# Performance work log

Measured on AMD Instinct MI355X. Metric: run time of the kernel, lower is better.

## Reference

```python
import jax, jax.numpy as jnp
import numpy as np


def _cross_head_proj(x, sw, qw1, qw2, kw1, kw2, qdd, kdd):
    # x: [B,N,T,S] attention logits/probs; sw: [N,N]
    # qw1/qw2: [B,T,I,N], kw1/kw2: [B,S,I,N] (I=2 dynamic rank), qdd: [B,T,N], kdd: [B,S,N]
    out = x + jnp.einsum('bnts,nm->bmts', x, sw)
    # low-rank dynamic mixing along query positions (sum over i reproduces the range(2) loop)
    qh = jnp.einsum('bnts,btin->bits', x, qw1)          # [B,I,T,S]
    out = out + jnp.einsum('bits,btin->bnts', qh, qw2)
    # low-rank dynamic mixing along key positions
    kh = jnp.einsum('bnts,bsin->bits', x, kw1)          # [B,I,T,S]
    out = out + jnp.einsum('bits,bsin->bnts', kh, kw2)
    # diagonal (per-head) dynamic terms
    out = out + x * jnp.transpose(qdd, (0, 2, 1))[:, :, :, None]   # [B,N,T,1]
    out = out + x * jnp.transpose(kdd, (0, 2, 1))[:, :, None, :]   # [B,N,1,S]
    return out


def setup_inputs() -> dict:
    key = jax.random.key(0)
    ks = jax.random.split(key, 18)
    B, N, T, S, D, I = 1, 32, 1024, 1024, 128, 2
    scale = 0.05  # dynamic weights come out of tanh/RMSnorm in the original; keep them small
    query = jax.random.normal(ks[0], (B, N, T, D), jnp.float32) * (D ** -0.5)
    k_ = jax.random.normal(ks[1], (B, N, S, D), jnp.float32)
    v_ = jax.random.normal(ks[2], (B, N, S, D), jnp.float32)
    neg = jnp.finfo(jnp.float32).min * 0.5  # matches make_causal_mask
    atten_mask = jnp.where(jnp.arange(S)[None, :] <= jnp.arange(T)[:, None], 0.0, neg).astype(jnp.float32)
    def dws(i0):
        return (
            jax.random.normal(ks[i0 + 0], (N, N), jnp.float32) * scale,
            jax.random.normal(ks[i0 + 1], (B, T, I, N), jnp.float32) * scale,
            jax.random.normal(ks[i0 + 2], (B, T, I, N), jnp.float32) * scale,
            jax.random.normal(ks[i0 + 3], (B, S, I, N), jnp.float32) * scale,
            jax.random.normal(ks[i0 + 4], (B, S, I, N), jnp.float32) * scale,
            jax.random.normal(ks[i0 + 5], (B, T, N), jnp.float32) * scale,
            jax.random.normal(ks[i0 + 6], (B, S, N), jnp.float32) * scale,
        )
    sw_pre, qw1_pre, qw2_pre, kw1_pre, kw2_pre, qdd_pre, kdd_pre = dws(3)
    sw_post, qw1_post, qw2_post, kw1_post, kw2_post, qdd_post, kdd_post = dws(10)
    return {
        'query': query, 'key': k_, 'value': v_, 'atten_mask': atten_mask,
        'sw_pre': sw_pre, 'qw1_pre': qw1_pre, 'qw2_pre': qw2_pre, 'kw1_pre': kw1_pre,
        'kw2_pre': kw2_pre, 'qdd_pre': qdd_pre, 'kdd_pre': kdd_pre,
        'sw_post': sw_post, 'qw1_post': qw1_post, 'qw2_post': qw2_post, 'kw1_post': kw1_post,
        'kw2_post': kw2_post, 'qdd_post': qdd_post, 'kdd_post': kdd_post,
    }


def reference(query, key, value, atten_mask,
              sw_pre, qw1_pre, qw2_pre, kw1_pre, kw2_pre, qdd_pre, kdd_pre,
              sw_post, qw1_post, qw2_post, kw1_post, kw2_post, qdd_post, kdd_post):
    # _atten_context: QK^T -> pre cross-head proj -> mask -> softmax -> post cross-head proj -> AV
    logits = jnp.einsum('bntd,bnsd->bnts', query, key)
    logits = _cross_head_proj(logits, sw_pre, qw1_pre, qw2_pre, kw1_pre, kw2_pre, qdd_pre, kdd_pre)
    logits = logits + atten_mask  # [T,S] broadcasts over [B,N,T,S]
    probs = jax.nn.softmax(logits, axis=-1)
    probs = _cross_head_proj(probs, sw_post, qw1_post, qw2_post, kw1_post, kw2_post, qdd_post, kdd_post)
    return jnp.einsum('bnts,bnsd->bntd', probs, value)
```

## Files before the change

kernel.cpp:

```cpp
#include <hip/hip_runtime.h>
#include <hip/hip_bf16.h>
#include <cstdint>
#include <cstddef>

#define T_DIM 1024
#define S_DIM 1024
#define N_HEADS 32
#define D_HEAD 128

typedef __attribute__((ext_vector_type(8))) short short8;
typedef __attribute__((ext_vector_type(4))) float floatx4;

__device__ inline int pack_bf16(float a, float b) {
    __hip_bfloat162 h = __float22bfloat162_rn(make_float2(a, b));
    int r; __builtin_memcpy(&r, &h, 4); return r;
}
__device__ inline ushort f2b(float x) {
    __hip_bfloat16 h = __float2bfloat16(x);
    ushort u; __builtin_memcpy(&u, &h, 2); return u;
}
__device__ inline float b2f(ushort u) {
    unsigned int v = ((unsigned int)u) << 16;
    float f; __builtin_memcpy(&f, &v, 4); return f;
}

__global__ __launch_bounds__(256) void tobf16(const float* __restrict__ Q,
                                              const float* __restrict__ K,
                                              ushort* __restrict__ Qb,
                                              ushort* __restrict__ Kb) {
    const size_t gid = (size_t)blockIdx.x * 256 + threadIdx.x;
    #pragma unroll
    for (int j = 0; j < 2; ++j) {
        size_t i = gid + (size_t)j * 524288;
        float4 q = ((const float4*)Q)[i];
        int2 qp; qp.x = pack_bf16(q.x, q.y); qp.y = pack_bf16(q.z, q.w);
        ((int2*)Qb)[i] = qp;
        float4 k = ((const float4*)K)[i];
        int2 kp; kp.x = pack_bf16(k.x, k.y); kp.y = pack_bf16(k.z, k.w);
        ((int2*)Kb)[i] = kp;
    }
}

__global__ __launch_bounds__(256) void vt_kernel(const float* __restrict__ V,
                                                 ushort* __restrict__ Vt) {
    const int s0 = blockIdx.x * 64;
    const int n  = blockIdx.y;
    __shared__ float lds[128 * 65];

    const int tid = threadIdx.x;
    const float* Vn = V + ((size_t)n * S_DIM + s0) * D_HEAD;

    #pragma unroll
    for (int it = 0; it < 8; ++it) {
        int idx = tid + it * 256;
        int d4 = idx & 31, s = idx >> 5;
        float4 v = *(const float4*)(Vn + (size_t)s * D_HEAD + d4 * 4);
        lds[(d4 * 4 + 0) * 65 + s] = v.x;
        lds[(d4 * 4 + 1) * 65 + s] = v.y;
        lds[(d4 * 4 + 2) * 65 + s] = v.z;
        lds[(d4 * 4 + 3) * 65 + s] = v.w;
    }
    __syncthreads();

    ushort* Vtn = Vt + (size_t)n * D_HEAD * S_DIM;
    #pragma unroll
    for (int it = 0; it < 4; ++it) {
        int idx = tid + it * 256;
        int sg = idx & 7, d = idx >> 3;
        const float* src = &lds[d * 65 + sg * 8];
        int4 o;
        o.x = pack_bf16(src[0], src[1]);
        o.y = pack_bf16(src[2], src[3]);
        o.z = pack_bf16(src[4], src[5]);
        o.w = pack_bf16(src[6], src[7]);
        *(int4*)&Vtn[(size_t)d * S_DIM + s0 + sg * 8] = o;
    }
}

__global__ __launch_bounds__(256, 2) void qk2(const ushort* __restrict__ Qb,
                                              const ushort* __restrict__ Kb,
                                              ushort* __restrict__ Lb) {
    const int bid  = blockIdx.x;
    const int xcd  = bid & 7;
    const int i    = bid >> 3;
    const int st   = i & 15;
    const int pair = (i >> 4) * 8 + xcd;
    const int n    = pair >> 4;
    const int tt   = pair & 15;
    if (st > tt) return;

    __shared__ int Qt[64 * 64];
    __shared__ int Kt[64 * 64];

    const int tid = threadIdx.x;
    const int wv = tid >> 6, ln = tid & 63;
    const int frow = ln & 15, quad = ln >> 4;

    const ushort* Qn = Qb + ((size_t)n * T_DIM + (size_t)tt * 64) * D_HEAD;
    const ushort* Kn = Kb + ((size_t)n * S_DIM + (size_t)st * 64) * D_HEAD;

    #pragma unroll
    for (int rep = 0; rep < 8; ++rep) {
        int idx = (tid + rep * 256) & 1023;
        int row = idx >> 4;
        int c   = idx & 15;
        int kb  = c >> 2, qw = c & 3;
        int dst = row * 64 + kb * 16 + ((qw * 4) ^ (4 * (row & 3)));
        if (rep < 4) {
            uint4 v = *(const uint4*)(Qn + (size_t)row * D_HEAD + c * 8);
            *(uint4*)&Qt[dst] = v;
        } else {
            uint4 v = *(const uint4*)(Kn + (size_t)row * D_HEAD + c * 8);
            *(uint4*)&Kt[dst] = v;
        }
    }
    __syncthreads();

    const int swz = 4 * (frow & 3);
    floatx4 acc[4] = {};
    #pragma unroll
    for (int kb = 0; kb < 4; ++kb) {
        const short8 af = *(const short8*)&Qt[(wv * 16 + frow) * 64 + kb * 16 + ((quad * 4) ^ swz)];
        #pragma unroll
        for (int si = 0; si < 4; ++si) {
            const short8 bf = *(const short8*)&Kt[(si * 16 + frow) * 64 + kb * 16 + ((quad * 4) ^ swz)];
            acc[si] = __builtin_amdgcn_mfma_f32_16x16x32_bf16(af, bf, acc[si], 0, 0, 0);
        }
    }
    __syncthreads();

    ushort* Ot = (ushort*)Qt;
    #pragma unroll
    for (int si = 0; si < 4; ++si)
        #pragma unroll
        for (int r = 0; r < 4; ++r)
            Ot[(wv * 16 + quad * 4 + r) * 72 + si * 16 + frow] = f2b(acc[si][r]);
    __syncthreads();

    #pragma unroll
    for (int it = 0; it < 2; ++it) {
        int idx = tid + it * 256;
        int row = idx >> 3, col = idx & 7;
        int4 v = *(const int4*)&Ot[row * 72 + col * 8];
        *(int4*)&Lb[((size_t)n * T_DIM + tt * 64 + row) * S_DIM + st * 64 + col * 8] = v;
    }
}

__global__ __launch_bounds__(256) void mat4_kernel(
        const float* __restrict__ sw_pre,  const float* __restrict__ qw1_pre,
        const float* __restrict__ qw2_pre, const float* __restrict__ qdd_pre,
        const float* __restrict__ kw1_pre, const float* __restrict__ kw2_pre,
        const float* __restrict__ kdd_pre,
        const float* __restrict__ sw_post,  const float* __restrict__ qw1_post,
        const float* __restrict__ qw2_post, const float* __restrict__ qdd_post,
        const float* __restrict__ kw1_post, const float* __restrict__ kw2_post,
        const float* __restrict__ kdd_post,
        ushort* __restrict__ mats) {
    const float *sw, *w1, *w2, *dd;
    float idadd;
    switch (blockIdx.y) {
        case 0:  sw = sw_pre;  w1 = qw1_pre;  w2 = qw2_pre;  dd = qdd_pre;  idadd = 1.0f; break;
        case 1:  sw = nullptr; w1 = kw1_pre;  w2 = kw2_pre;  dd = kdd_pre;  idadd = 0.0f; break;
        case 2:  sw = sw_post; w1 = qw1_post; w2 = qw2_post; dd = qdd_post; idadd = 1.0f; break;
        default: sw = nullptr; w1 = kw1_post; w2 = kw2_post; dd = kdd_post; idadd = 0.0f; break;
    }
    ushort* out = mats + (size_t)blockIdx.y * 1024 * 1024;

    const int t = blockIdx.x;
    const int tid = threadIdx.x;
    const int m = tid >> 3;
    const int n0 = (tid & 7) * 4;

    const float w2m0 = w2[t * 64 + m];
    const float w2m1 = w2[t * 64 + 32 + m];
    const float ddm  = dd[t * 32 + m];

    float v[4];
    #pragma unroll
    for (int j = 0; j < 4; ++j) {
        int n = n0 + j;
        float r = w1[t * 64 + n] * w2m0 + w1[t * 64 + 32 + n] * w2m1;
        if (sw) r += sw[n * 32 + m];
        if (n == m) r += idadd + ddm;
        v[j] = r;
    }
    int p0 = pack_bf16(v[0], v[1]);
    int p1 = pack_bf16(v[2], v[3]);
    int2 st = make_int2(p0, p1);
    *(int2*)&out[(size_t)t * 1024 + m * 32 + n0] = st;
}

template<bool SM>
__global__ __launch_bounds__(256, 4) void proj6(ushort* __restrict__ Lb,
                                                const ushort* __restrict__ Cmat,
                                                const ushort* __restrict__ Kmat,
                                                const float2* __restrict__ stats2,
                                                float2* __restrict__ pstat) {
    const int bid = blockIdx.y * 64 + blockIdx.x;
    const int xcd = bid & 7;
    const int idx = bid >> 3;
    const int ty  = ((idx >> 6) << 3) + xcd;
    const int sx  = idx & 63;

    const int s0 = sx * 16;
    const int t0 = ty * 16;
    if (s0 > t0 + 15) return;

    __shared__ __align__(16) ushort Xs[16 * 648];
    __shared__ __align__(16) float  Kp[16 * 260];

    const int tid = threadIdx.x;
    const int wv = tid >> 6, ln = tid & 63;
    const int frow = ln & 15, quad = ln >> 4;

    #pragma unroll
    for (int it = 0; it < 4; ++it) {
        int slot = tid + it * 256;
        int c    = slot & 1;
        int row  = slot >> 1;
        int nn   = row >> 4, tl = row & 15;
        uint4 ld = *(const uint4*)(Lb + ((size_t)nn * T_DIM + t0 + tl) * S_DIM + s0 + c * 8);
        ushort u[8];
        u[0] = (ushort)(ld.x & 0xffff);  u[1] = (ushort)(ld.x >> 16);
        u[2] = (ushort)(ld.y & 0xffff);  u[3] = (ushort)(ld.y >> 16);
        u[4] = (ushort)(ld.z & 0xffff);  u[5] = (ushort)(ld.z >> 16);
        u[6] = (ushort)(ld.w & 0xffff);  u[7] = (ushort)(ld.w >> 16);
        if (SM) {
            const float2 ms = stats2[(t0 + tl) * 32 + nn];
            const int tG = t0 + tl, sbase = s0 + c * 8;
            #pragma unroll
            for (int j = 0; j < 8; ++j) {
                float x = (sbase + j <= tG) ? __expf(b2f(u[j]) - ms.x) * ms.y : 0.0f;
                u[j] = f2b(x);
            }
        }
        ushort* xp = &Xs[tl * 648 + (c * 8) * 40 + nn];
        #pragma unroll
        for (int j = 0; j < 8; ++j) xp[j * 40] = u[j];
    }
    __syncthreads();

    #pragma unroll
    for (int mh = 0; mh < 2; ++mh) {
        #pragma unroll
        for (int k = 0; k < 4; ++k) {
            const int sl = wv * 4 + k;
            const short8 af = *(const short8*)(Kmat + (size_t)(s0 + sl) * 1024 + (mh * 16 + frow) * 32 + quad * 8);
            const short8 bf = *(const short8*)&Xs[frow * 648 + sl * 40 + quad * 8];
            floatx4 z = {0.f, 0.f, 0.f, 0.f};
            floatx4 d = __builtin_amdgcn_mfma_f32_16x16x32_bf16(af, bf, z, 0, 0, 0);
            *(floatx4*)&Kp[frow * 260 + sl * 16 + quad * 4] = d;
        }
        __syncthreads();

        #pragma unroll
        for (int i = 0; i < 4; ++i) {
            const int tl = wv * 4 + i;
            const int tg = t0 + tl;
            const short8 bf = *(const short8*)(Cmat + (size_t)tg * 1024 + (mh * 16 + frow) * 32 + quad * 8);
            const short8 af = *(const short8*)&Xs[tl * 648 + frow * 40 + quad * 8];
            floatx4 z = {0.f, 0.f, 0.f, 0.f};
            floatx4 d = __builtin_amdgcn_mfma_f32_16x16x32_bf16(af, bf, z, 0, 0, 0);
            float v[4];
            float lm = -INFINITY, lsum = 0.0f;
            #pragma unroll
            for (int r = 0; r < 4; ++r) {
                const int sl = quad * 4 + r;
                float val = d[r] + Kp[tl * 260 + sl * 16 + frow];
                const bool ok = (s0 + sl <= tg);
                v[r] = ok ? val : 0.0f;
                if (!SM) lm = fmaxf(lm, ok ? val : -INFINITY);
            }
            if (!SM) {
                #pragma unroll
                for (int r = 0; r < 4; ++r) {
                    const int sl = quad * 4 + r;
                    if (s0 + sl <= tg) lsum += __expf(v[r] - lm);
                }
                #pragma unroll
                for (int off = 16; off <= 32; off <<= 1) {
                    float om = __shfl_xor(lm, off);
                    float os = __shfl_xor(lsum, off);
                    float nm = fmaxf(lm, om);
                    float a = (lm > -1e37f) ? lsum * __expf(lm - nm) : 0.0f;
                    float b = (om > -1e37f) ? os   * __expf(om - nm) : 0.0f;
                    lm = nm; lsum = a + b;
                }
                if (quad == 0)
                    pstat[((size_t)tg * 64 + sx) * 32 + mh * 16 + frow] = make_float2(lm, lsum);
            }
            uint2 stv;
            stv.x = (unsigned)pack_bf16(v[0], v[1]);
            stv.y = (unsigned)pack_bf16(v[2], v[3]);
            *(uint2*)&Lb[((size_t)(mh * 16 + frow) * T_DIM + tg) * S_DIM + s0 + quad * 4] = stv;
        }
        __syncthreads();
    }
}

__global__ __launch_bounds__(256) void statreduce(const float2* __restrict__ pstat,
                                                  float2* __restrict__ stats2) {
    const int t = blockIdx.x;
    const int ty = t >> 4;
    const int total = (ty + 1) * 32;
    __shared__ float sm[32][65];
    __shared__ float ss[32][65];

    const int tid = threadIdx.x;
    for (int base = 0; base < total; base += 256) {
        int idx = base + tid;
        if (idx < total) {
            float2 p = pstat[(size_t)t * 2048 + idx];
            sm[idx & 31][idx >> 5] = p.x;
            ss[idx & 31][idx >> 5] = p.y;
        }
    }
    __syncthreads();

    const int n = tid >> 3, j = tid & 7;
    float m = -INFINITY, s = 0.0f;
    for (int sx = j; sx <= ty; sx += 8) {
        float om = sm[n][sx], os = ss[n][sx];
        float nm = fmaxf(m, om);
        float a = (m  > -1e37f) ? s  * __expf(m  - nm) : 0.0f;
        float b = (om > -1e37f) ? os * __expf(om - nm) : 0.0f;
        m = nm; s = a + b;
    }
    #pragma unroll
    for (int off = 1; off < 8; off <<= 1) {
        float om = __shfl_xor(m, off);
        float os = __shfl_xor(s, off);
        float nm = fmaxf(m, om);
        float a = (m  > -1e37f) ? s  * __expf(m  - nm) : 0.0f;
        float b = (om > -1e37f) ? os * __expf(om - nm) : 0.0f;
        m = nm; s = a + b;
    }
    if (j == 0) stats2[t * 32 + n] = make_float2(m, 1.0f / s);
}

__global__ __launch_bounds__(256, 3) void av4(const ushort* __restrict__ P,
                                              const ushort* __restrict__ Vt,
                                              float* __restrict__ O) {
    const int tid = threadIdx.x;
    const int wv = tid >> 6, ln = tid & 63;
    const int frow = ln & 15, quad = ln >> 4;
    const int n  = blockIdx.x;
    const int tt = 31 - blockIdx.y;
    const int t0 = tt * 32;

    __shared__ ushort red[4][32][136];

    const ushort* Pn  = P  + ((size_t)n * T_DIM + t0) * S_DIM;
    const ushort* Vtn = Vt + (size_t)n * D_HEAD * S_DIM;

    const int nsteps  = tt + 1;
    const int nclean0 = t0 >> 5;
    const int nclean1 = (t0 + 16) >> 5;

    floatx4 acc[2][8] = {};
    for (int sb = wv; sb < nsteps; sb += 4) {
        const int scol = sb * 32 + quad * 8;
        short8 a0 = *(const short8*)(Pn + (size_t)frow * S_DIM + scol);
        short8 a1 = *(const short8*)(Pn + (size_t)(16 + frow) * S_DIM + scol);
        if (sb >= nclean0) {
            const int tg = t0 + frow;
            #pragma unroll
            for (int j = 0; j < 8; ++j)
                if (scol + j > tg) a0[j] = 0;
        }
        if (sb >= nclean1) {
            const int tg = t0 + 16 + frow;
            #pragma unroll
            for (int j = 0; j < 8; ++j)
                if (scol + j > tg) a1[j] = 0;
        }
        #pragma unroll
        for (int dc = 0; dc < 8; ++dc) {
            const short8 b = *(const short8*)(Vtn + (size_t)(dc * 16 + frow) * S_DIM + sb * 32 + quad * 8);
            acc[0][dc] = __builtin_amdgcn_mfma_f32_16x16x32_bf16(a0, b, acc[0][dc], 0, 0, 0);
            acc[1][dc] = __builtin_amdgcn_mfma_f32_16x16x32_bf16(a1, b, acc[1][dc], 0, 0, 0);
        }
    }

    #pragma unroll
    for (int tq = 0; tq < 2; ++tq)
        #pragma unroll
        for (int dc = 0; dc < 8; ++dc)
            #pragma unroll
            for (int r = 0; r < 4; ++r)
                red[wv][tq * 16 + quad * 4 + r][dc * 16 + frow] = f2b(acc[tq][dc][r]);
    __syncthreads();

    #pragma unroll
    for (int it = 0; it < 4; ++it) {
        int idx = tid + it * 256;
        int d4 = idx & 31, tr = idx >> 5;
        float4 v;
        v.x = b2f(red[0][tr][d4 * 4 + 0]) + b2f(red[1][tr][d4 * 4 + 0]) + b2f(red[2][tr][d4 * 4 + 0]) + b2f(red[3][tr][d4 * 4 + 0]);
        v.y = b2f(red[0][tr][d4 * 4 + 1]) + b2f(red[1][tr][d4 * 4 + 1]) + b2f(red[2][tr][d4 * 4 + 1]) + b2f(red[3][tr][d4 * 4 + 1]);
        v.z = b2f(red[0][tr][d4 * 4 + 2]) + b2f(red[1][tr][d4 * 4 + 2]) + b2f(red[2][tr][d4 * 4 + 2]) + b2f(red[3][tr][d4 * 4 + 2]);
        v.w = b2f(red[0][tr][d4 * 4 + 3]) + b2f(red[1][tr][d4 * 4 + 3]) + b2f(red[2][tr][d4 * 4 + 3]) + b2f(red[3][tr][d4 * 4 + 3]);
        *(float4*)&O[((size_t)n * T_DIM + t0 + tr) * D_HEAD + d4 * 4] = v;
    }
}

extern "C" void kernel_launch(void* const* d_in, const int* in_sizes, int n_in,
                              void* d_out, int out_size, void* d_ws, size_t ws_size,
                              hipStream_t stream) {
    const float* Q    = (const float*)d_in[0];
    const float* K    = (const float*)d_in[1];
    const float* V    = (const float*)d_in[2];
    const float* sw_pre  = (const float*)d_in[4];
    const float* qw1_pre = (const float*)d_in[5];
    const float* qw2_pre = (const float*)d_in[6];
    const float* kw1_pre = (const float*)d_in[7];
    const float* kw2_pre = (const float*)d_in[8];
    const float* qdd_pre = (const float*)d_in[9];
    const float* kdd_pre = (const float*)d_in[10];
    const float* sw_post  = (const float*)d_in[11];
    const float* qw1_post = (const float*)d_in[12];
    const float* qw2_post = (const float*)d_in[13];
    const float* kw1_post = (const float*)d_in[14];
    const float* kw2_post = (const float*)d_in[15];
    const float* qdd_post = (const float*)d_in[16];
    const float* kdd_post = (const float*)d_in[17];

    ushort* Lb = (ushort*)d_ws;
    ushort* Vt = (ushort*)((char*)d_ws + (size_t)64 * 1024 * 1024);
    ushort* Qb = (ushort*)((char*)d_ws + (size_t)72 * 1024 * 1024);
    ushort* Kb = (ushort*)((char*)d_ws + (size_t)80 * 1024 * 1024);
    float2* pstat = (float2*)((char*)d_ws + (size_t)96 * 1024 * 1024);
    float*  O  = (float*)d_out;

    ushort* mats  = (ushort*)d_out;
    ushort* Cpre  = mats + 0 * 1024 * 1024;
    ushort* Kpre  = mats + 1 * 1024 * 1024;
    ushort* Cpost = mats + 2 * 1024 * 1024;
    ushort* Kpost = mats + 3 * 1024 * 1024;
    float2* stats2 = (float2*)((char*)d_out + (size_t)8 * 1024 * 1024);

    mat4_kernel<<<dim3(1024, 4), 256, 0, stream>>>(
        sw_pre, qw1_pre, qw2_pre, qdd_pre, kw1_pre, kw2_pre, kdd_pre,
        sw_post, qw1_post, qw2_post, qdd_post, kw1_post, kw2_post, kdd_post, mats);
    tobf16<<<dim3(2048), 256, 0, stream>>>(Q, K, Qb, Kb);
    vt_kernel<<<dim3(16, 32), 256, 0, stream>>>(V, Vt);

    qk2<<<dim3(8192), 256, 0, stream>>>(Qb, Kb, Lb);
    proj6<false><<<dim3(64, 64), 256, 0, stream>>>(Lb, Cpre, Kpre, nullptr, pstat);
    statreduce<<<dim3(1024), 256, 0, stream>>>(pstat, stats2);
    proj6<true><<<dim3(64, 64), 256, 0, stream>>>(Lb, Cpost, Kpost, stats2, nullptr);
    av4<<<dim3(32, 32), 256, 0, stream>>>(Lb, Vt, O);
}
```

Measured before the change: 244.6 us.

## Merge prep kernels into one launch and compute two K tiles per QK block

The three preprocessing kernels (mixing-matrix build, Q/K bf16 conversion, V transpose) become a single launch that dispatches on block index. This removes two kernel launches and their gaps. The QK^T kernel now has each block reuse its staged Q tile across two adjacent 64-wide K tiles, which halves the grid and the Q reloads. In exchange it uses more LDS per block (three tiles) and adds a conditional second tile at the causal diagonal, with the occupancy hint raised to 3.

```diff
diff --git a/kernel.cpp b/kernel.cpp
--- a/kernel.cpp
+++ b/kernel.cpp
@@ -24,129 +24,9 @@
     float f; __builtin_memcpy(&f, &v, 4); return f;
 }
 
-__global__ __launch_bounds__(256) void tobf16(const float* __restrict__ Q,
-                                              const float* __restrict__ K,
-                                              ushort* __restrict__ Qb,
-                                              ushort* __restrict__ Kb) {
-    const size_t gid = (size_t)blockIdx.x * 256 + threadIdx.x;
-    #pragma unroll
-    for (int j = 0; j < 2; ++j) {
-        size_t i = gid + (size_t)j * 524288;
-        float4 q = ((const float4*)Q)[i];
-        int2 qp; qp.x = pack_bf16(q.x, q.y); qp.y = pack_bf16(q.z, q.w);
-        ((int2*)Qb)[i] = qp;
-        float4 k = ((const float4*)K)[i];
-        int2 kp; kp.x = pack_bf16(k.x, k.y); kp.y = pack_bf16(k.z, k.w);
-        ((int2*)Kb)[i] = kp;
-    }
-}
-
-__global__ __launch_bounds__(256) void vt_kernel(const float* __restrict__ V,
-                                                 ushort* __restrict__ Vt) {
-    const int s0 = blockIdx.x * 64;
-    const int n  = blockIdx.y;
-    __shared__ float lds[128 * 65];
-
-    const int tid = threadIdx.x;
-    const float* Vn = V + ((size_t)n * S_DIM + s0) * D_HEAD;
-
-    #pragma unroll
-    for (int it = 0; it < 8; ++it) {
-        int idx = tid + it * 256;
-        int d4 = idx & 31, s = idx >> 5;
-        float4 v = *(const float4*)(Vn + (size_t)s * D_HEAD + d4 * 4);
-        lds[(d4 * 4 + 0) * 65 + s] = v.x;
-        lds[(d4 * 4 + 1) * 65 + s] = v.y;
-        lds[(d4 * 4 + 2) * 65 + s] = v.z;
-        lds[(d4 * 4 + 3) * 65 + s] = v.w;
-    }
-    __syncthreads();
-
-    ushort* Vtn = Vt + (size_t)n * D_HEAD * S_DIM;
-    #pragma unroll
-    for (int it = 0; it < 4; ++it) {
-        int idx = tid + it * 256;
-        int sg = idx & 7, d = idx >> 3;
-        const float* src = &lds[d * 65 + sg * 8];
-        int4 o;
-        o.x = pack_bf16(src[0], src[1]);
-        o.y = pack_bf16(src[2], src[3]);
-        o.z = pack_bf16(src[4], src[5]);
-        o.w = pack_bf16(src[6], src[7]);
-        *(int4*)&Vtn[(size_t)d * S_DIM + s0 + sg * 8] = o;
-    }
-}
-
-__global__ __launch_bounds__(256, 2) void qk2(const ushort* __restrict__ Qb,
-                                              const ushort* __restrict__ Kb,
-                                              ushort* __restrict__ Lb) {
-    const int bid  = blockIdx.x;
-    const int xcd  = bid & 7;
-    const int i    = bid >> 3;
-    const int st   = i & 15;
-    const int pair = (i >> 4) * 8 + xcd;
-    const int n    = pair >> 4;
-    const int tt   = pair & 15;
-    if (st > tt) return;
-
-    __shared__ int Qt[64 * 64];
-    __shared__ int Kt[64 * 64];
-
-    const int tid = threadIdx.x;
-    const int wv = tid >> 6, ln = tid & 63;
-    const int frow = ln & 15, quad = ln >> 4;
-
-    const ushort* Qn = Qb + ((size_t)n * T_DIM + (size_t)tt * 64) * D_HEAD;
-    const ushort* Kn = Kb + ((size_t)n * S_DIM + (size_t)st * 64) * D_HEAD;
-
-    #pragma unroll
-    for (int rep = 0; rep < 8; ++rep) {
-        int idx = (tid + rep * 256) & 1023;
-        int row = idx >> 4;
-        int c   = idx & 15;
-        int kb  = c >> 2, qw = c & 3;
-        int dst = row * 64 + kb * 16 + ((qw * 4) ^ (4 * (row & 3)));
-        if (rep < 4) {
-            uint4 v = *(const uint4*)(Qn + (size_t)row * D_HEAD + c * 8);
-            *(uint4*)&Qt[dst] = v;
-        } else {
-            uint4 v = *(const uint4*)(Kn + (size_t)row * D_HEAD + c * 8);
-            *(uint4*)&Kt[dst] = v;
-        }
-    }
-    __syncthreads();
-
-    const int swz = 4 * (frow & 3);
-    floatx4 acc[4] = {};
-    #pragma unroll
-    for (int kb = 0; kb < 4; ++kb) {
-        const short8 af = *(const short8*)&Qt[(wv * 16 + frow) * 64 + kb * 16 + ((quad * 4) ^ swz)];
-        #pragma unroll
-        for (int si = 0; si < 4; ++si) {
-            const short8 bf = *(const short8*)&Kt[(si * 16 + frow) * 64 + kb * 16 + ((quad * 4) ^ swz)];
-            acc[si] = __builtin_amdgcn_mfma_f32_16x16x32_bf16(af, bf, acc[si], 0, 0, 0);
-        }
-    }
-    __syncthreads();
-
-    ushort* Ot = (ushort*)Qt;
-    #pragma unroll
-    for (int si = 0; si < 4; ++si)
-        #pragma unroll
-        for (int r = 0; r < 4; ++r)
-            Ot[(wv * 16 + quad * 4 + r) * 72 + si * 16 + frow] = f2b(acc[si][r]);
-    __syncthreads();
-
-    #pragma unroll
-    for (int it = 0; it < 2; ++it) {
-        int idx = tid + it * 256;
-        int row = idx >> 3, col = idx & 7;
-        int4 v = *(const int4*)&Ot[row * 72 + col * 8];
-        *(int4*)&Lb[((size_t)n * T_DIM + tt * 64 + row) * S_DIM + st * 64 + col * 8] = v;
-    }
-}
-
-__global__ __launch_bounds__(256) void mat4_kernel(
+__global__ __launch_bounds__(256) void prep(
+        const float* __restrict__ Q, const float* __restrict__ K,
+        const float* __restrict__ V,
         const float* __restrict__ sw_pre,  const float* __restrict__ qw1_pre,
         const float* __restrict__ qw2_pre, const float* __restrict__ qdd_pre,
         const float* __restrict__ kw1_pre, const float* __restrict__ kw2_pre,
@@ -155,39 +35,163 @@
         const float* __restrict__ qw2_post, const float* __restrict__ qdd_post,
         const float* __restrict__ kw1_post, const float* __restrict__ kw2_post,
         const float* __restrict__ kdd_post,
-        ushort* __restrict__ mats) {
-    const float *sw, *w1, *w2, *dd;
-    float idadd;
-    switch (blockIdx.y) {
-        case 0:  sw = sw_pre;  w1 = qw1_pre;  w2 = qw2_pre;  dd = qdd_pre;  idadd = 1.0f; break;
-        case 1:  sw = nullptr; w1 = kw1_pre;  w2 = kw2_pre;  dd = kdd_pre;  idadd = 0.0f; break;
-        case 2:  sw = sw_post; w1 = qw1_post; w2 = qw2_post; dd = qdd_post; idadd = 1.0f; break;
-        default: sw = nullptr; w1 = kw1_post; w2 = kw2_post; dd = kdd_post; idadd = 0.0f; break;
-    }
-    ushort* out = mats + (size_t)blockIdx.y * 1024 * 1024;
-
-    const int t = blockIdx.x;
+        ushort* __restrict__ mats, ushort* __restrict__ Qb,
+        ushort* __restrict__ Kb, ushort* __restrict__ Vt) {
+    __shared__ float lds[128 * 65];
+    const int bid = blockIdx.x;
     const int tid = threadIdx.x;
-    const int m = tid >> 3;
-    const int n0 = (tid & 7) * 4;
-
-    const float w2m0 = w2[t * 64 + m];
-    const float w2m1 = w2[t * 64 + 32 + m];
-    const float ddm  = dd[t * 32 + m];
-
-    float v[4];
-    #pragma unroll
-    for (int j = 0; j < 4; ++j) {
-        int n = n0 + j;
-        float r = w1[t * 64 + n] * w2m0 + w1[t * 64 + 32 + n] * w2m1;
-        if (sw) r += sw[n * 32 + m];
-        if (n == m) r += idadd + ddm;
-        v[j] = r;
-    }
-    int p0 = pack_bf16(v[0], v[1]);
-    int p1 = pack_bf16(v[2], v[3]);
-    int2 st = make_int2(p0, p1);
-    *(int2*)&out[(size_t)t * 1024 + m * 32 + n0] = st;
+
+    if (bid < 4096) {
+        const int fam = bid & 3;
+        const int t   = bid >> 2;
+        const float *sw, *w1, *w2, *dd;
+        float idadd;
+        switch (fam) {
+            case 0:  sw = sw_pre;  w1 = qw1_pre;  w2 = qw2_pre;  dd = qdd_pre;  idadd = 1.0f; break;
+            case 1:  sw = nullptr; w1 = kw1_pre;  w2 = kw2_pre;  dd = kdd_pre;  idadd = 0.0f; break;
+            case 2:  sw = sw_post; w1 = qw1_post; w2 = qw2_post; dd = qdd_post; idadd = 1.0f; break;
+            default: sw = nullptr; w1 = kw1_post; w2 = kw2_post; dd = kdd_post; idadd = 0.0f; break;
+        }
+        ushort* out = mats + (size_t)fam * 1024 * 1024;
+        const int m = tid >> 3;
+        const int n0 = (tid & 7) * 4;
+        const float w2m0 = w2[t * 64 + m];
+        const float w2m1 = w2[t * 64 + 32 + m];
+        const float ddm  = dd[t * 32 + m];
+        float v[4];
+        #pragma unroll
+        for (int j = 0; j < 4; ++j) {
+            int n = n0 + j;
+            float r = w1[t * 64 + n] * w2m0 + w1[t * 64 + 32 + n] * w2m1;
+            if (sw) r += sw[n * 32 + m];
+            if (n == m) r += idadd + ddm;
+            v[j] = r;
+        }
+        int2 st = make_int2(pack_bf16(v[0], v[1]), pack_bf16(v[2], v[3]));
+        *(int2*)&out[(size_t)t * 1024 + m * 32 + n0] = st;
+    } else if (bid < 6144) {
+        const size_t gid = (size_t)(bid - 4096) * 256 + tid;
+        #pragma unroll
+        for (int j = 0; j < 2; ++j) {
+            size_t i = gid + (size_t)j * 524288;
+            float4 q = ((const float4*)Q)[i];
+            int2 qp; qp.x = pack_bf16(q.x, q.y); qp.y = pack_bf16(q.z, q.w);
+            ((int2*)Qb)[i] = qp;
+            float4 k = ((const float4*)K)[i];
+            int2 kp; kp.x = pack_bf16(k.x, k.y); kp.y = pack_bf16(k.z, k.w);
+            ((int2*)Kb)[i] = kp;
+        }
+    } else {
+        const int vb = bid - 6144;
+        const int s0 = (vb & 15) * 64;
+        const int n  = vb >> 4;
+        const float* Vn = V + ((size_t)n * S_DIM + s0) * D_HEAD;
+        #pragma unroll
+        for (int it = 0; it < 8; ++it) {
+            int idx = tid + it * 256;
+            int d4 = idx & 31, s = idx >> 5;
+            float4 v = *(const float4*)(Vn + (size_t)s * D_HEAD + d4 * 4);
+            lds[(d4 * 4 + 0) * 65 + s] = v.x;
+            lds[(d4 * 4 + 1) * 65 + s] = v.y;
+            lds[(d4 * 4 + 2) * 65 + s] = v.z;
+            lds[(d4 * 4 + 3) * 65 + s] = v.w;
+        }
+        __syncthreads();
+        ushort* Vtn = Vt + (size_t)n * D_HEAD * S_DIM;
+        #pragma unroll
+        for (int it = 0; it < 4; ++it) {
+            int idx = tid + it * 256;
+            int sg = idx & 7, d = idx >> 3;
+            const float* src = &lds[d * 65 + sg * 8];
+            int4 o;
+            o.x = pack_bf16(src[0], src[1]);
+            o.y = pack_bf16(src[2], src[3]);
+            o.z = pack_bf16(src[4], src[5]);
+            o.w = pack_bf16(src[6], src[7]);
+            *(int4*)&Vtn[(size_t)d * S_DIM + s0 + sg * 8] = o;
+        }
+    }
+}
+
+__global__ __launch_bounds__(256, 3) void qk3(const ushort* __restrict__ Qb,
+                                              const ushort* __restrict__ Kb,
+                                              ushort* __restrict__ Lb) {
+    const int bid  = blockIdx.x;
+    const int xcd  = bid & 7;
+    const int i    = bid >> 3;
+    const int sp   = i & 7;
+    const int pair = (i >> 3) * 8 + xcd;
+    const int n    = pair >> 4;
+    const int tt   = pair & 15;
+    const int st0  = sp * 2;
+    if (st0 > tt) return;
+    const bool two = (st0 + 1 <= tt);
+
+    __shared__ int Qt[64 * 64];
+    __shared__ int Kt0[64 * 64];
+    __shared__ int Kt1[64 * 64];
+
+    const int tid = threadIdx.x;
+    const int wv = tid >> 6, ln = tid & 63;
+    const int frow = ln & 15, quad = ln >> 4;
+
+    const ushort* Qn  = Qb + ((size_t)n * T_DIM + (size_t)tt * 64) * D_HEAD;
+    const ushort* Kn0 = Kb + ((size_t)n * S_DIM + (size_t)st0 * 64) * D_HEAD;
+    const ushort* Kn1 = Kn0 + (size_t)64 * D_HEAD;
+
+    #pragma unroll
+    for (int rep = 0; rep < 4; ++rep) {
+        int idx = tid + rep * 256;
+        int row = idx >> 4;
+        int c   = idx & 15;
+        int dst = row * 64 + (c >> 2) * 16 + (((c & 3) * 4) ^ (4 * (row & 3)));
+        *(uint4*)&Qt[dst]  = *(const uint4*)(Qn  + (size_t)row * D_HEAD + c * 8);
+        *(uint4*)&Kt0[dst] = *(const uint4*)(Kn0 + (size_t)row * D_HEAD + c * 8);
+        if (two)
+            *(uint4*)&Kt1[dst] = *(const uint4*)(Kn1 + (size_t)row * D_HEAD + c * 8);
+    }
+    __syncthreads();
+
+    const int swz = 4 * (frow & 3);
+    floatx4 acc0[4] = {};
+    floatx4 acc1[4] = {};
+    #pragma unroll
+    for (int kb = 0; kb < 4; ++kb) {
+        const short8 af = *(const short8*)&Qt[(wv * 16 + frow) * 64 + kb * 16 + ((quad * 4) ^ swz)];
+        #pragma unroll
+        for (int si = 0; si < 4; ++si) {
+            const int off = (si * 16 + frow) * 64 + kb * 16 + ((quad * 4) ^ swz);
+            const short8 bf0 = *(const short8*)&Kt0[off];
+            acc0[si] = __builtin_amdgcn_mfma_f32_16x16x32_bf16(af, bf0, acc0[si], 0, 0, 0);
+            if (two) {
+                const short8 bf1 = *(const short8*)&Kt1[off];
+                acc1[si] = __builtin_amdgcn_mfma_f32_16x16x32_bf16(af, bf1, acc1[si], 0, 0, 0);
+            }
+        }
+    }
+    __syncthreads();
+
+    ushort* Ot0 = (ushort*)Qt;
+    ushort* Ot1 = (ushort*)Kt0;
+    #pragma unroll
+    for (int si = 0; si < 4; ++si)
+        #pragma unroll
+        for (int r = 0; r < 4; ++r) {
+            Ot0[(wv * 16 + quad * 4 + r) * 72 + si * 16 + frow] = f2b(acc0[si][r]);
+            if (two)
+                Ot1[(wv * 16 + quad * 4 + r) * 72 + si * 16 + frow] = f2b(acc1[si][r]);
+        }
+    __syncthreads();
+
+    #pragma unroll
+    for (int it = 0; it < 2; ++it) {
+        int idx = tid + it * 256;
+        int row = idx >> 3, col = idx & 7;
+        ushort* dst = &Lb[((size_t)n * T_DIM + tt * 64 + row) * S_DIM + st0 * 64 + col * 8];
+        *(int4*)dst = *(const int4*)&Ot0[row * 72 + col * 8];
+        if (two)
+            *(int4*)(dst + 64) = *(const int4*)&Ot1[row * 72 + col * 8];
+    }
 }
 
 template<bool SM>
@@ -439,13 +443,13 @@
     ushort* Kpost = mats + 3 * 1024 * 1024;
     float2* stats2 = (float2*)((char*)d_out + (size_t)8 * 1024 * 1024);
 
-    mat4_kernel<<<dim3(1024, 4), 256, 0, stream>>>(
+    prep<<<dim3(6656), 256, 0, stream>>>(
+        Q, K, V,
         sw_pre, qw1_pre, qw2_pre, qdd_pre, kw1_pre, kw2_pre, kdd_pre,
-        sw_post, qw1_post, qw2_post, qdd_post, kw1_post, kw2_post, kdd_post, mats);
-    tobf16<<<dim3(2048), 256, 0, stream>>>(Q, K, Qb, Kb);
-    vt_kernel<<<dim3(16, 32), 256, 0, stream>>>(V, Vt);
-
-    qk2<<<dim3(8192), 256, 0, stream>>>(Qb, Kb, Lb);
+        sw_post, qw1_post, qw2_post, qdd_post, kw1_post, kw2_post, kdd_post,
+        mats, Qb, Kb, Vt);
+
+    qk3<<<dim3(4096), 256, 0, stream>>>(Qb, Kb, Lb);
     proj6<false><<<dim3(64, 64), 256, 0, stream>>>(Lb, Cpre, Kpre, nullptr, pstat);
     statreduce<<<dim3(1024), 256, 0, stream>>>(pstat, stats2);
     proj6<true><<<dim3(64, 64), 256, 0, stream>>>(Lb, Cpost, Kpost, stats2, nullptr);
```

Result: slower. 254.0 us (+3.9%).
